# Performance work log

Measured on AMD Instinct MI355X. Metric: run time of the kernel, lower is better.

## Reference

```python
import jax, jax.numpy as jnp
import numpy as np

B, S, D = 1, 2048, 2048
H, G = 32, 8            # n_heads, n_groups
HPG = H // G            # heads per group = 4
HD = D // H             # head_dim = 64


def setup_inputs() -> dict:
    key = jax.random.key(0)
    ks = jax.random.split(key, 5)
    w_scale = 0.02
    return {
        "x":  jax.random.normal(ks[0], (B, S, D), dtype=jnp.float32),
        "Wq": jax.random.normal(ks[1], (D, D), dtype=jnp.float32) * w_scale,
        "bq": jnp.zeros((D,), dtype=jnp.float32),
        "Wk": jax.random.normal(ks[2], (G * HD, D), dtype=jnp.float32) * w_scale,
        "bk": jnp.zeros((G * HD,), dtype=jnp.float32),
        "Wv": jax.random.normal(ks[3], (G * HD, D), dtype=jnp.float32) * w_scale,
        "bv": jnp.zeros((G * HD,), dtype=jnp.float32),
        "Wo": jax.random.normal(ks[4], (D, D), dtype=jnp.float32) * w_scale,
        "bo": jnp.zeros((D,), dtype=jnp.float32),
    }


def reference(x, Wq, bq, Wk, bk, Wv, bv, Wo, bo):
    b, n, _ = x.shape
    # projections (torch Linear: y = x @ W.T + b)
    q = x @ Wq.T + bq                              # [b, n, D]
    k = x @ Wk.T + bk                              # [b, n, G*HD]
    v = x @ Wv.T + bv                              # [b, n, G*HD]
    # q: [b, n, H, HD] -> [b, H, n, HD] -> split heads as (g h): [b, G, HPG, n, HD]
    q = q.reshape(b, n, H, HD).transpose(0, 2, 1, 3).reshape(b, G, HPG, n, HD)
    k = k.reshape(b, n, G, HD).transpose(0, 2, 1, 3)   # [b, G, n, HD]
    v = v.reshape(b, n, G, HD).transpose(0, 2, 1, 3)   # [b, G, n, HD]
    scale = 1.0 / jnp.sqrt(jnp.asarray(HD, dtype=q.dtype))
    attn_score = jnp.einsum('bghnd,bgsd->bghns', q, k) * scale
    attn_prob = jax.nn.softmax(attn_score, axis=-1)
    out = jnp.einsum('bghns,bgsd->bghnd', attn_prob, v)   # [b, G, HPG, n, HD]
    # faithful to original: rearrange 'b g h n d -> b n (h g d)' (h-major, g-minor)
    out = out.transpose(0, 3, 2, 1, 4).reshape(b, n, HPG * G * HD)
    return out @ Wo.T + bo
```

## Files before the change

kernel.cpp:

```cpp
#include <hip/hip_runtime.h>
#include <hip/hip_bf16.h>

constexpr int kS   = 2048;
constexpr int kD   = 2048;
constexpr int kG   = 8;
constexpr int kHD  = 64;
constexpr int kGHD = 512;
constexpr int kNQKV = kD + 2 * kGHD;

constexpr float kQScale = 0.125f * 1.4426950408889634f;

typedef __attribute__((ext_vector_type(8)))  _Float16 f16x8;
typedef __attribute__((ext_vector_type(4)))  float    f32x4;
typedef __attribute__((ext_vector_type(16))) float    f32x16;
typedef __attribute__((ext_vector_type(4)))  unsigned int u32x4;

__device__ __forceinline__ ushort f2h(float x) {
    return __builtin_bit_cast(ushort, (_Float16)x);
}
__device__ __forceinline__ float fast_exp2(float x) {
    return __builtin_amdgcn_exp2f(x);
}
__device__ __forceinline__ unsigned int pkrtz(float a, float b) {
    auto r = __builtin_amdgcn_cvt_pkrtz(a, b);
    return __builtin_bit_cast(unsigned int, r);
}

__global__ __launch_bounds__(256) void cvt_f16(
    const float* __restrict__ in, ushort* __restrict__ out, int n, float scale)
{
    const int i = (blockIdx.x * 256 + threadIdx.x) * 4;
    if (i >= n) return;
    const float4 x = *(const float4*)&in[i];
    ushort4 o;
    o.x = f2h(x.x * scale); o.y = f2h(x.y * scale);
    o.z = f2h(x.z * scale); o.w = f2h(x.w * scale);
    *(ushort4*)&out[i] = o;
}

__global__ __launch_bounds__(256) void prep_bias(
    const float* __restrict__ bq, const float* __restrict__ bk,
    const float* __restrict__ bv, float* __restrict__ bqkv)
{
    const int i = blockIdx.x * 256 + threadIdx.x;
    if (i < kD)             bqkv[i] = bq[i] * kQScale;
    else if (i < kD + kGHD) bqkv[i] = bk[i - kD];
    else if (i < kNQKV)     bqkv[i] = bv[i - kD - kGHD];
}

__device__ __forceinline__ int xcd_swizzle(int orig, int nwg) {
    const int cpx = nwg >> 3;
    return (orig & 7) * cpx + (orig >> 3);
}

#define GEMM_PRELUDE(Aptr, Bptr)                                              \
    const int bid  = xcd_swizzle(blockIdx.x, gridDim.x);                      \
    const int m0   = (bid / gridX) * 128;                                     \
    const int n0   = (bid % gridX) * 128;                                     \
    const int tid  = threadIdx.x;                                             \
    const int w    = tid >> 6;                                                \
    const int lane = tid & 63;                                                \
    const int wm   = w >> 2;                                                  \
    const int wn   = w & 3;                                                   \
    const int fr   = lane & 15;                                               \
    const int kq   = lane >> 4;                                               \
    const int srow = w * 16 + (lane >> 2);                                    \
    const int sslot = ((lane & 3) ^ ((lane >> 3) & 3)) * 8;                   \
    const ushort* gA = (Aptr) + (size_t)(m0 + srow) * K + sslot;              \
    const ushort* gB = (Bptr) + (size_t)(n0 + srow) * K + sslot;              \
    const int pslot = (kq ^ ((fr >> 1) & 3)) * 8;                             \
    f32x4 acc[4][2];                                                          \
    _Pragma("unroll")                                                         \
    for (int mi = 0; mi < 4; ++mi)                                            \
        _Pragma("unroll")                                                     \
        for (int ni = 0; ni < 2; ++ni) {                                      \
            f32x4 z = {0.f, 0.f, 0.f, 0.f};                                   \
            acc[mi][ni] = z;                                                  \
        }

#define GEMM_STAGE(buf, k0)                                                   \
    do {                                                                      \
        __builtin_amdgcn_global_load_lds(                                     \
            (const __attribute__((address_space(1))) void*)(gA + (k0)),       \
            (__attribute__((address_space(3))) void*)&lds[buf][0][w * 512],   \
            16, 0, 0);                                                        \
        __builtin_amdgcn_global_load_lds(                                     \
            (const __attribute__((address_space(1))) void*)(gB + (k0)),       \
            (__attribute__((address_space(3))) void*)&lds[buf][1][w * 512],   \
            16, 0, 0);                                                        \
    } while (0)

#define GEMM_KLOOP(MFMA_BODY)                                                 \
    GEMM_STAGE(0, 0);                                                         \
    __syncthreads();                                                          \
    int cur = 0;                                                              \
    for (int k0 = 0; k0 < K; k0 += 32) {                                      \
        if (k0 + 32 < K) GEMM_STAGE(cur ^ 1, k0 + 32);                        \
        f16x8 af[4], bf[2];                                                   \
        _Pragma("unroll")                                                     \
        for (int f = 0; f < 4; ++f)                                           \
            af[f] = *(const f16x8*)&lds[cur][0][(wm * 64 + f * 16 + fr) * 32 + pslot]; \
        _Pragma("unroll")                                                     \
        for (int f = 0; f < 2; ++f)                                           \
            bf[f] = *(const f16x8*)&lds[cur][1][(wn * 32 + f * 16 + fr) * 32 + pslot]; \
        __builtin_amdgcn_s_setprio(1);                                        \
        MFMA_BODY                                                             \
        __builtin_amdgcn_s_setprio(0);                                        \
        __syncthreads();                                                      \
        cur ^= 1;                                                             \
    }

__global__ __launch_bounds__(512) void gemm_qkv(
    const ushort* __restrict__ Af, const ushort* __restrict__ Bf,
    const float* __restrict__ bias,
    ushort* __restrict__ qb16, ushort* __restrict__ kb16, ushort* __restrict__ vt16,
    int K, int gridX)
{
    __shared__ ushort lds[2][2][128 * 32];

    GEMM_PRELUDE(Af, Bf)
    GEMM_KLOOP(
        _Pragma("unroll")
        for (int mi = 0; mi < 4; ++mi)
            _Pragma("unroll")
            for (int ni = 0; ni < 2; ++ni)
                acc[mi][ni] = __builtin_amdgcn_mfma_f32_16x16x32_f16(
                    af[mi], bf[ni], acc[mi][ni], 0, 0, 0);
    )

    const int seg = (n0 < kD) ? 0 : (n0 < kD + kGHD) ? 1 : 2;
    #pragma unroll
    for (int ni = 0; ni < 2; ++ni) {
        const int ncol = n0 + wn * 32 + ni * 16 + fr;
        const float bv = bias[ncol];
        #pragma unroll
        for (int mi = 0; mi < 4; ++mi) {
            #pragma unroll
            for (int i = 0; i < 4; ++i) {
                const int row = m0 + wm * 64 + mi * 16 + kq * 4 + i;
                const ushort u = f2h(acc[mi][ni][i] + bv);
                if (seg == 0)      qb16[(size_t)row * kD   + ncol]              = u;
                else if (seg == 1) kb16[(size_t)row * kGHD + (ncol - kD)]       = u;
                else               vt16[(size_t)(ncol - kD - kGHD) * kS + row]  = u;
            }
        }
    }
}

__global__ __launch_bounds__(512) void gemm_o(
    const ushort* __restrict__ Af, const ushort* __restrict__ Bf,
    const float* __restrict__ bias, float* __restrict__ C, int K, int N, int gridX)
{
    __shared__ ushort lds[2][2][128 * 32];

    GEMM_PRELUDE(Af, Bf)
    GEMM_KLOOP(
        _Pragma("unroll")
        for (int mi = 0; mi < 4; ++mi)
            _Pragma("unroll")
            for (int ni = 0; ni < 2; ++ni)
                acc[mi][ni] = __builtin_amdgcn_mfma_f32_16x16x32_f16(
                    af[mi], bf[ni], acc[mi][ni], 0, 0, 0);
    )

    #pragma unroll
    for (int ni = 0; ni < 2; ++ni) {
        const int ncol = n0 + wn * 32 + ni * 16 + fr;
        const float bv = bias[ncol];
        #pragma unroll
        for (int mi = 0; mi < 4; ++mi)
            #pragma unroll
            for (int i = 0; i < 4; ++i) {
                const int row = m0 + wm * 64 + mi * 16 + kq * 4 + i;
                C[(size_t)row * N + ncol] = acc[mi][ni][i] + bv;
            }
    }
}

__global__ __launch_bounds__(256) void gqa_attn_mfma(
    const ushort* __restrict__ qb,
    const ushort* __restrict__ kb,
    const ushort* __restrict__ vt,
    ushort* __restrict__ oh)
{
    __shared__ ushort Kt[2][64 * 64];
    __shared__ ushort Vt[2][64 * 64];

    const int g    = blockIdx.y;
    const int q0   = blockIdx.x * 32;
    const int tid  = threadIdx.x;
    const int w    = tid >> 6;
    const int lane = tid & 63;
    const int ql   = lane & 31;
    const int hi   = lane >> 5;
    const int h    = g * 4 + w;

    const int r0 = w * 16 + (lane >> 3);
    const int ss = (lane & 7) ^ (r0 & 7);

#define ATTN_STAGE(buf, t)                                                         \
    do {                                                                           \
        __builtin_amdgcn_global_load_lds(                                          \
            (const __attribute__((address_space(1))) void*)                       \
                (kb + (size_t)((t) + r0) * kGHD + g * kHD + ss * 8),               \
            (__attribute__((address_space(3))) void*)(Kt[buf] + (w * 16) * 64),    \
            16, 0, 0);                                                             \
        __builtin_amdgcn_global_load_lds(                                          \
            (const __attribute__((address_space(1))) void*)                       \
                (kb + (size_t)((t) + r0 + 8) * kGHD + g * kHD + ss * 8),           \
            (__attribute__((address_space(3))) void*)(Kt[buf] + (w * 16 + 8) * 64),\
            16, 0, 0);                                                             \
        __builtin_amdgcn_global_load_lds(                                          \
            (const __attribute__((address_space(1))) void*)                       \
                (vt + (size_t)(g * kHD + r0) * kS + (t) + ss * 8),                 \
            (__attribute__((address_space(3))) void*)(Vt[buf] + (w * 16) * 64),    \
            16, 0, 0);                                                             \
        __builtin_amdgcn_global_load_lds(                                          \
            (const __attribute__((address_space(1))) void*)                       \
                (vt + (size_t)(g * kHD + r0 + 8) * kS + (t) + ss * 8),             \
            (__attribute__((address_space(3))) void*)(Vt[buf] + (w * 16 + 8) * 64),\
            16, 0, 0);                                                             \
    } while (0)

    ATTN_STAGE(0, 0);

    f16x8 qf[4];
    #pragma unroll
    for (int ks = 0; ks < 4; ++ks)
        qf[ks] = *(const f16x8*)&qb[(size_t)(q0 + ql) * kD + h * kHD + ks * 16 + hi * 8];

    float mrow = -1e30f, lrow = 0.f;
    f32x16 oacc[2];
    #pragma unroll
    for (int db = 0; db < 2; ++db)
        #pragma unroll
        for (int r = 0; r < 16; ++r) oacc[db][r] = 0.f;

    int cur = 0;
    for (int t = 0; t < kS; t += 64) {
        __syncthreads();

        if (t + 64 < kS) ATTN_STAGE(cur ^ 1, t + 64);

        f32x16 sc[2];
        #pragma unroll
        for (int kb2 = 0; kb2 < 2; ++kb2)
            #pragma unroll
            for (int r = 0; r < 16; ++r) sc[kb2][r] = 0.f;

        #pragma unroll
        for (int kb2 = 0; kb2 < 2; ++kb2) {
            #pragma unroll
            for (int ks = 0; ks < 4; ++ks) {
                const f16x8 kf = *(const f16x8*)&Kt[cur][(kb2 * 32 + ql) * 64
                                     + (((2 * ks + hi) ^ (ql & 7)) * 8)];
                __builtin_amdgcn_s_setprio(1);
                sc[kb2] = __builtin_amdgcn_mfma_f32_32x32x16_f16(
                    kf, qf[ks], sc[kb2], 0, 0, 0);
                __builtin_amdgcn_s_setprio(0);
            }
        }

        float mt = sc[0][0];
        #pragma unroll
        for (int kb2 = 0; kb2 < 2; ++kb2)
            #pragma unroll
            for (int r = 0; r < 16; ++r) mt = fmaxf(mt, sc[kb2][r]);
        mt = fmaxf(mt, __shfl_xor(mt, 32));

        if (__any(mt > mrow + 11.5f)) {
            const float mnew = (mt > mrow + 11.5f) ? mt : mrow;
            const float c = fast_exp2(mrow - mnew);
            lrow *= c;
            mrow = mnew;
            #pragma unroll
            for (int db = 0; db < 2; ++db)
                #pragma unroll
                for (int r = 0; r < 16; ++r) oacc[db][r] *= c;
        }

        float ps = 0.f;
        #pragma unroll
        for (int kb2 = 0; kb2 < 2; ++kb2)
            #pragma unroll
            for (int r = 0; r < 16; ++r) {
                const float p = fast_exp2(sc[kb2][r] - mrow);
                sc[kb2][r] = p;
                ps += p;
            }
        ps += __shfl_xor(ps, 32);
        lrow += ps;

        #pragma unroll
        for (int kb2 = 0; kb2 < 2; ++kb2) {
            #pragma unroll
            for (int ks = 0; ks < 2; ++ks) {
                unsigned int a0 = pkrtz(sc[kb2][8 * ks + 0], sc[kb2][8 * ks + 1]);
                unsigned int a1 = pkrtz(sc[kb2][8 * ks + 2], sc[kb2][8 * ks + 3]);
                unsigned int b0 = pkrtz(sc[kb2][8 * ks + 4], sc[kb2][8 * ks + 5]);
                unsigned int b1 = pkrtz(sc[kb2][8 * ks + 6], sc[kb2][8 * ks + 7]);
                asm volatile("v_permlane32_swap_b32 %0, %1"
                             : "+v"(a0), "+v"(b0));
                asm volatile("v_permlane32_swap_b32 %0, %1"
                             : "+v"(a1), "+v"(b1));
                const u32x4 pu = {a0, a1, b0, b1};
                const f16x8 pf = __builtin_bit_cast(f16x8, pu);
                #pragma unroll
                for (int db = 0; db < 2; ++db) {
                    const f16x8 vf = *(const f16x8*)&Vt[cur][(db * 32 + ql) * 64
                                         + (((4 * kb2 + 2 * ks + hi) ^ (ql & 7)) * 8)];
                    __builtin_amdgcn_s_setprio(1);
                    oacc[db] = __builtin_amdgcn_mfma_f32_32x32x16_f16(
                        vf, pf, oacc[db], 0, 0, 0);
                    __builtin_amdgcn_s_setprio(0);
                }
            }
        }
        cur ^= 1;
    }

    const float inv = 1.f / lrow;
    const size_t rowbase = (size_t)(q0 + ql) * kD + w * kGHD + g * kHD;
    #pragma unroll
    for (int db = 0; db < 2; ++db) {
        #pragma unroll
        for (int rr = 0; rr < 4; ++rr) {
            ushort4 o4;
            o4.x = f2h(oacc[db][rr * 4 + 0] * inv);
            o4.y = f2h(oacc[db][rr * 4 + 1] * inv);
            o4.z = f2h(oacc[db][rr * 4 + 2] * inv);
            o4.w = f2h(oacc[db][rr * 4 + 3] * inv);
            *(ushort4*)&oh[rowbase + db * 32 + rr * 8 + hi * 4] = o4;
        }
    }
#undef ATTN_STAGE
}

extern "C" void kernel_launch(void* const* d_in, const int* in_sizes, int n_in,
                              void* d_out, int out_size, void* d_ws, size_t ws_size,
                              hipStream_t stream)
{
    const float* x  = (const float*)d_in[0];
    const float* Wq = (const float*)d_in[1];
    const float* bq = (const float*)d_in[2];
    const float* Wk = (const float*)d_in[3];
    const float* bk = (const float*)d_in[4];
    const float* Wv = (const float*)d_in[5];
    const float* bv = (const float*)d_in[6];
    const float* Wo = (const float*)d_in[7];
    const float* bo = (const float*)d_in[8];
    float* out = (float*)d_out;

    char* p = (char*)d_ws;
    ushort* xf    = (ushort*)p; p += (size_t)kS * kD * 2;
    ushort* wqkvf = (ushort*)p; p += (size_t)kNQKV * kD * 2;
    ushort* wof   = (ushort*)p; p += (size_t)kD * kD * 2;
    float*  bqkv  = (float*)p;  p += 16384;
    ushort* qb16  = (ushort*)p; p += (size_t)kS * kD * 2;
    ushort* kb16  = (ushort*)p; p += (size_t)kS * kGHD * 2;
    ushort* vt16  = (ushort*)p; p += (size_t)kGHD * kS * 2;
    ushort* aoh   = (ushort*)p;

    cvt_f16<<<kS * kD / 1024, 256, 0, stream>>>(x, xf, kS * kD, 1.f);
    cvt_f16<<<kD * kD / 1024, 256, 0, stream>>>(Wq, wqkvf, kD * kD, kQScale);
    cvt_f16<<<kGHD * kD / 1024, 256, 0, stream>>>(Wk, wqkvf + (size_t)kD * kD, kGHD * kD, 1.f);
    cvt_f16<<<kGHD * kD / 1024, 256, 0, stream>>>(
        Wv, wqkvf + (size_t)(kD + kGHD) * kD, kGHD * kD, 1.f);
    cvt_f16<<<kD * kD / 1024, 256, 0, stream>>>(Wo, wof, kD * kD, 1.f);
    prep_bias<<<(kNQKV + 255) / 256, 256, 0, stream>>>(bq, bk, bv, bqkv);

    gemm_qkv<<<(kNQKV / 128) * (kS / 128), 512, 0, stream>>>(
        xf, wqkvf, bqkv, qb16, kb16, vt16, kD, kNQKV / 128);

    gqa_attn_mfma<<<dim3(kS / 32, kG), 256, 0, stream>>>(qb16, kb16, vt16, aoh);

    gemm_o<<<(kD / 128) * (kS / 128), 512, 0, stream>>>(
        aoh, wof, bo, out, kD, kD, kD / 128);
}
```

Baseline: 159.4 us.

## Split attention KV sequence across two warp halves with in-block merge

Doubles the attention block to 512 threads, with each half of the warps processing half of the key/value sequence for the same queries, using separate double-buffered LDS tiles. After the loop, the second half writes its partial output accumulators and running max/sum to shared memory, and the first half merges them with log-sum-exp rescaling before writing. This aims to raise parallelism and latency hiding, since the grid has only 512 blocks, at the cost of doubled LDS, an extra merge pass and idle warps during the epilogue.

```diff
diff --git a/kernel.cpp b/kernel.cpp
--- a/kernel.cpp
+++ b/kernel.cpp
@@ -177,48 +177,51 @@
     }
 }
 
-__global__ __launch_bounds__(256) void gqa_attn_mfma(
+__global__ __launch_bounds__(512) void gqa_attn_mfma(
     const ushort* __restrict__ qb,
     const ushort* __restrict__ kb,
     const ushort* __restrict__ vt,
     ushort* __restrict__ oh)
 {
-    __shared__ ushort Kt[2][64 * 64];
-    __shared__ ushort Vt[2][64 * 64];
+    __shared__ ushort Kt[2][2][64 * 64];
+    __shared__ ushort Vt[2][2][64 * 64];
 
     const int g    = blockIdx.y;
     const int q0   = blockIdx.x * 32;
     const int tid  = threadIdx.x;
     const int w    = tid >> 6;
     const int lane = tid & 63;
+    const int hw   = w & 3;
+    const int half = w >> 2;
     const int ql   = lane & 31;
     const int hi   = lane >> 5;
-    const int h    = g * 4 + w;
-
-    const int r0 = w * 16 + (lane >> 3);
+    const int h    = g * 4 + hw;
+    const int tbase = half * (kS / 2);
+
+    const int r0 = hw * 16 + (lane >> 3);
     const int ss = (lane & 7) ^ (r0 & 7);
 
 #define ATTN_STAGE(buf, t)                                                         \
     do {                                                                           \
         __builtin_amdgcn_global_load_lds(                                          \
             (const __attribute__((address_space(1))) void*)                       \
-                (kb + (size_t)((t) + r0) * kGHD + g * kHD + ss * 8),               \
-            (__attribute__((address_space(3))) void*)(Kt[buf] + (w * 16) * 64),    \
+                (kb + (size_t)(tbase + (t) + r0) * kGHD + g * kHD + ss * 8),       \
+            (__attribute__((address_space(3))) void*)(&Kt[half][buf][(hw * 16) * 64]), \
             16, 0, 0);                                                             \
         __builtin_amdgcn_global_load_lds(                                          \
             (const __attribute__((address_space(1))) void*)                       \
-                (kb + (size_t)((t) + r0 + 8) * kGHD + g * kHD + ss * 8),           \
-            (__attribute__((address_space(3))) void*)(Kt[buf] + (w * 16 + 8) * 64),\
+                (kb + (size_t)(tbase + (t) + r0 + 8) * kGHD + g * kHD + ss * 8),   \
+            (__attribute__((address_space(3))) void*)(&Kt[half][buf][(hw * 16 + 8) * 64]), \
             16, 0, 0);                                                             \
         __builtin_amdgcn_global_load_lds(                                          \
             (const __attribute__((address_space(1))) void*)                       \
-                (vt + (size_t)(g * kHD + r0) * kS + (t) + ss * 8),                 \
-            (__attribute__((address_space(3))) void*)(Vt[buf] + (w * 16) * 64),    \
+                (vt + (size_t)(g * kHD + r0) * kS + tbase + (t) + ss * 8),         \
+            (__attribute__((address_space(3))) void*)(&Vt[half][buf][(hw * 16) * 64]), \
             16, 0, 0);                                                             \
         __builtin_amdgcn_global_load_lds(                                          \
             (const __attribute__((address_space(1))) void*)                       \
-                (vt + (size_t)(g * kHD + r0 + 8) * kS + (t) + ss * 8),             \
-            (__attribute__((address_space(3))) void*)(Vt[buf] + (w * 16 + 8) * 64),\
+                (vt + (size_t)(g * kHD + r0 + 8) * kS + tbase + (t) + ss * 8),     \
+            (__attribute__((address_space(3))) void*)(&Vt[half][buf][(hw * 16 + 8) * 64]), \
             16, 0, 0);                                                             \
     } while (0)
 
@@ -237,10 +240,10 @@
         for (int r = 0; r < 16; ++r) oacc[db][r] = 0.f;
 
     int cur = 0;
-    for (int t = 0; t < kS; t += 64) {
+    for (int t = 0; t < kS / 2; t += 64) {
         __syncthreads();
 
-        if (t + 64 < kS) ATTN_STAGE(cur ^ 1, t + 64);
+        if (t + 64 < kS / 2) ATTN_STAGE(cur ^ 1, t + 64);
 
         f32x16 sc[2];
         #pragma unroll
@@ -252,7 +255,7 @@
         for (int kb2 = 0; kb2 < 2; ++kb2) {
             #pragma unroll
             for (int ks = 0; ks < 4; ++ks) {
-                const f16x8 kf = *(const f16x8*)&Kt[cur][(kb2 * 32 + ql) * 64
+                const f16x8 kf = *(const f16x8*)&Kt[half][cur][(kb2 * 32 + ql) * 64
                                      + (((2 * ks + hi) ^ (ql & 7)) * 8)];
                 __builtin_amdgcn_s_setprio(1);
                 sc[kb2] = __builtin_amdgcn_mfma_f32_32x32x16_f16(
@@ -307,7 +310,7 @@
                 const f16x8 pf = __builtin_bit_cast(f16x8, pu);
                 #pragma unroll
                 for (int db = 0; db < 2; ++db) {
-                    const f16x8 vf = *(const f16x8*)&Vt[cur][(db * 32 + ql) * 64
+                    const f16x8 vf = *(const f16x8*)&Vt[half][cur][(db * 32 + ql) * 64
                                          + (((4 * kb2 + 2 * ks + hi) ^ (ql & 7)) * 8)];
                     __builtin_amdgcn_s_setprio(1);
                     oacc[db] = __builtin_amdgcn_mfma_f32_32x32x16_f16(
@@ -318,22 +321,45 @@
         }
         cur ^= 1;
     }
-
-    const float inv = 1.f / lrow;
-    const size_t rowbase = (size_t)(q0 + ql) * kD + w * kGHD + g * kHD;
-    #pragma unroll
-    for (int db = 0; db < 2; ++db) {
-        #pragma unroll
-        for (int rr = 0; rr < 4; ++rr) {
-            ushort4 o4;
-            o4.x = f2h(oacc[db][rr * 4 + 0] * inv);
-            o4.y = f2h(oacc[db][rr * 4 + 1] * inv);
-            o4.z = f2h(oacc[db][rr * 4 + 2] * inv);
-            o4.w = f2h(oacc[db][rr * 4 + 3] * inv);
-            *(ushort4*)&oh[rowbase + db * 32 + rr * 8 + hi * 4] = o4;
-        }
-    }
 #undef ATTN_STAGE
+
+    __syncthreads();
+    float* ox  = (float*)(&Kt[0][0][0]);
+    float* mlx = (float*)(&Vt[0][0][0]);
+    const int idx = hw * 64 + lane;
+
+    if (half == 1) {
+        #pragma unroll
+        for (int db = 0; db < 2; ++db)
+            #pragma unroll
+            for (int r = 0; r < 16; ++r)
+                ox[(db * 16 + r) * 256 + idx] = oacc[db][r];
+        mlx[idx]       = mrow;
+        mlx[256 + idx] = lrow;
+    }
+    __syncthreads();
+
+    if (half == 0) {
+        const float m2 = mlx[idx];
+        const float l2 = mlx[256 + idx];
+        const float mm = fmaxf(mrow, m2);
+        const float c1 = fast_exp2(mrow - mm);
+        const float c2 = fast_exp2(m2 - mm);
+        const float inv = 1.f / (lrow * c1 + l2 * c2);
+        const size_t rowbase = (size_t)(q0 + ql) * kD + hw * kGHD + g * kHD;
+        #pragma unroll
+        for (int db = 0; db < 2; ++db) {
+            #pragma unroll
+            for (int rr = 0; rr < 4; ++rr) {
+                ushort4 o4;
+                o4.x = f2h((oacc[db][rr * 4 + 0] * c1 + ox[(db * 16 + rr * 4 + 0) * 256 + idx] * c2) * inv);
+                o4.y = f2h((oacc[db][rr * 4 + 1] * c1 + ox[(db * 16 + rr * 4 + 1) * 256 + idx] * c2) * inv);
+                o4.z = f2h((oacc[db][rr * 4 + 2] * c1 + ox[(db * 16 + rr * 4 + 2) * 256 + idx] * c2) * inv);
+                o4.w = f2h((oacc[db][rr * 4 + 3] * c1 + ox[(db * 16 + rr * 4 + 3) * 256 + idx] * c2) * inv);
+                *(ushort4*)&oh[rowbase + db * 32 + rr * 8 + hi * 4] = o4;
+            }
+        }
+    }
 }
 
 extern "C" void kernel_launch(void* const* d_in, const int* in_sizes, int n_in,
@@ -372,7 +398,7 @@
     gemm_qkv<<<(kNQKV / 128) * (kS / 128), 512, 0, stream>>>(
         xf, wqkvf, bqkv, qb16, kb16, vt16, kD, kNQKV / 128);
 
-    gqa_attn_mfma<<<dim3(kS / 32, kG), 256, 0, stream>>>(qb16, kb16, vt16, aoh);
+    gqa_attn_mfma<<<dim3(kS / 32, kG), 512, 0, stream>>>(qb16, kb16, vt16, aoh);
 
     gemm_o<<<(kD / 128) * (kS / 128), 512, 0, stream>>>(
         aoh, wof, bo, out, kD, kD, kD / 128);
```

After: 149.0 us. 1.07x faster.
